# Performance work log

Hardware: AMD Instinct MI355X
Metric: run time of the kernel (lower is better)

## Reference

```python
import jax, jax.numpy as jnp
import numpy as np

B, C_IN, C_OUT, L = 16, 128, 128, 1024
DK, DV, H = 32, 32, 8
SCALE = DK ** (-0.5)


def setup_inputs() -> dict:
    key = jax.random.key(0)
    ks = jax.random.split(key, 7)
    qkv_dim = H * (2 * DK + DV)
    # Conv1d with kernel_size=1 == per-position linear; store weights as (out, in)
    return {
        "x": jax.random.normal(ks[0], (B, C_IN, L), dtype=jnp.float32),
        "w_qkv": jax.random.normal(ks[1], (qkv_dim, C_IN), dtype=jnp.float32) * (C_IN ** -0.5),
        "b_qkv": jax.random.normal(ks[2], (qkv_dim,), dtype=jnp.float32) * 0.02,
        "w_o": jax.random.normal(ks[3], (C_OUT, H * DV), dtype=jnp.float32) * ((H * DV) ** -0.5),
        "b_o": jax.random.normal(ks[4], (C_OUT,), dtype=jnp.float32) * 0.02,
        "w_res": jax.random.normal(ks[5], (C_OUT, C_IN), dtype=jnp.float32) * (C_IN ** -0.5),
        "b_res": jax.random.normal(ks[6], (C_OUT,), dtype=jnp.float32) * 0.02,
    }


def reference(x, w_qkv, b_qkv, w_o, b_o, w_res, b_res):
    batch, _, seq = x.shape
    # qkv projection (1x1 conv): (B, H*(2dk+dv), L)
    qkv = jnp.einsum("oc,bcl->bol", w_qkv, x) + b_qkv[:, None]
    qkv = qkv.reshape(batch, H, 2 * DK + DV, seq)
    q = qkv[:, :, :DK]                 # (B, H, dk, L)
    k = qkv[:, :, DK:2 * DK]           # (B, H, dk, L)
    v = qkv[:, :, 2 * DK:]             # (B, H, dv, L)
    # logits = scale * q^T k : (B, H, L, L)
    logits = SCALE * jnp.einsum("bhds,bhdt->bhst", q, k)
    weights = jax.nn.softmax(logits, axis=-1)
    # z_i = (weights @ v^T)^T : (B, H, dv, L)
    z = jnp.einsum("bhst,bhdt->bhds", weights, v)
    z = z.reshape(batch, H * DV, seq)
    out = jnp.einsum("oc,bcl->bol", w_o, z) + b_o[:, None]
    out = out + jnp.einsum("oc,bcl->bol", w_res, x) + b_res[:, None]
    return out
```

## Files before the change

### kernel.cpp

```cpp
#include <hip/hip_runtime.h>

#define B_    16
#define L_    1024
#define H_    8
#define QSCALE 0.25510940349191965f

typedef __attribute__((ext_vector_type(8))) short bf16x8;
typedef __attribute__((ext_vector_type(4))) float f32x4;
typedef unsigned short u16t;

__device__ inline u16t f2bf(float f) {
    unsigned u = __float_as_uint(f);
    u = (u + 0x7FFF + ((u >> 16) & 1)) >> 16;
    return (u16t)u;
}
__device__ inline unsigned f2bf_pk(float a, float b) {
    unsigned ua = __float_as_uint(a);
    unsigned ub = __float_as_uint(b);
    ua = (ua + 0x7FFF + ((ua >> 16) & 1)) >> 16;
    ub = (ub + 0x7FFF + ((ub >> 16) & 1)) >> 16;
    return ua | (ub << 16);
}
__device__ inline uint2 f2bf_pk4(float a, float b, float c, float d) {
    uint2 u; u.x = f2bf_pk(a, b); u.y = f2bf_pk(c, d); return u;
}
__device__ inline unsigned trunc_pk(float f0, float f1) {
    return __builtin_amdgcn_perm(__float_as_uint(f1), __float_as_uint(f0), 0x07060302u);
}
__device__ inline void async16(const u16t* g, u16t* l) {
    __builtin_amdgcn_global_load_lds(
        (const __attribute__((address_space(1))) unsigned int*)g,
        (__attribute__((address_space(3))) unsigned int*)l, 16, 0, 0);
}

__global__ __launch_bounds__(256) void prep_kernel(
    const float* __restrict__ x, const float* __restrict__ w_qkv,
    const float* __restrict__ w_o, const float* __restrict__ w_res,
    u16t* __restrict__ xbT, u16t* __restrict__ wqb,
    u16t* __restrict__ wob, u16t* __restrict__ wrb)
{
    const int tid = threadIdx.x;
    if (blockIdx.z == 0) {
        __shared__ u16t T[64][144];
        const int b = blockIdx.y, l0 = blockIdx.x * 64;
#pragma unroll
        for (int i = 0; i < 8; i++) {
            const int c = i * 16 + (tid >> 4);
            const int l = (tid & 15) * 4;
            const float4 v = *(const float4*)(x + ((long)b * 128 + c) * 1024 + l0 + l);
            T[l + 0][c] = f2bf(v.x);
            T[l + 1][c] = f2bf(v.y);
            T[l + 2][c] = f2bf(v.z);
            T[l + 3][c] = f2bf(v.w);
        }
        __syncthreads();
#pragma unroll
        for (int i = 0; i < 4; i++) {
            const int l  = i * 16 + (tid >> 4);
            const int c0 = (tid & 15) * 8;
            *(uint4*)(xbT + ((long)b * 1024 + l0 + l) * 128 + c0) = *(const uint4*)&T[l][c0];
        }
    } else {
        const int idx = blockIdx.y * 16 + blockIdx.x;
        if (idx >= 144) return;
        const int f = idx * 1024 + tid * 4;
        const float* src; u16t* dst; int off;
        if (f < 98304)       { src = w_qkv; dst = wqb; off = f; }
        else if (f < 131072) { src = w_o;   dst = wob; off = f - 98304; }
        else                 { src = w_res; dst = wrb; off = f - 131072; }
        const float4 v = *(const float4*)(src + off);
        *(uint2*)(dst + off) = f2bf_pk4(v.x, v.y, v.z, v.w);
    }
}

__global__ __launch_bounds__(256) void qkv_gemm_kernel(
    const u16t* __restrict__ wqb, const u16t* __restrict__ xbT,
    const float* __restrict__ b_qkv,
    u16t* __restrict__ qT, u16t* __restrict__ kF, u16t* __restrict__ vF)
{
    __shared__ __align__(16) u16t Ws[96 * 136];

    const int lblk = blockIdx.x * 128;
    const int bh = blockIdx.y;
    const int b = bh >> 3, h = bh & 7;
    const int tid = threadIdx.x, lane = tid & 63, wv = tid >> 6;
    const int l15 = lane & 15, quad = lane >> 4;
    const int lw = lblk + wv * 32;

    {
        const u16t* wsrc = wqb + (long)h * 96 * 128;
#pragma unroll
        for (int i = 0; i < 6; i++) {
            const int g = tid + i * 256;
            const int row = g >> 4, col = g & 15;
            const uint4 w = *(const uint4*)(wsrc + g * 8);
            *(uint4*)&Ws[row * 136 + col * 8] = w;
        }
    }

    bf16x8 bfr[4][2];
    {
        const u16t* xr0 = xbT + ((long)b * 1024 + lw + l15) * 128 + quad * 8;
        const u16t* xr1 = xr0 + 16 * 128;
#pragma unroll
        for (int ks = 0; ks < 4; ks++) {
            bfr[ks][0] = *(const bf16x8*)(xr0 + ks * 32);
            bfr[ks][1] = *(const bf16x8*)(xr1 + ks * 32);
        }
    }
    __syncthreads();

    f32x4 acc[6][2];
#pragma unroll
    for (int mi = 0; mi < 6; mi++)
#pragma unroll
        for (int ni = 0; ni < 2; ni++) acc[mi][ni] = (f32x4)0.f;

#pragma unroll
    for (int ks = 0; ks < 4; ks++) {
#pragma unroll
        for (int mi = 0; mi < 6; mi++) {
            const bf16x8 af = *(const bf16x8*)&Ws[(mi * 16 + l15) * 136 + ks * 32 + quad * 8];
            acc[mi][0] = __builtin_amdgcn_mfma_f32_16x16x32_bf16(af, bfr[ks][0], acc[mi][0], 0, 0, 0);
            acc[mi][1] = __builtin_amdgcn_mfma_f32_16x16x32_bf16(af, bfr[ks][1], acc[mi][1], 0, 0, 0);
        }
    }

    const long bh_ = bh;
#pragma unroll
    for (int mi = 0; mi < 6; mi++) {
        float bias[4];
#pragma unroll
        for (int r = 0; r < 4; r++) bias[r] = b_qkv[h * 96 + mi * 16 + quad * 4 + r];
#pragma unroll
        for (int ni = 0; ni < 2; ni++) {
            const int l = lw + ni * 16 + l15;
            const f32x4 a = acc[mi][ni];
            if (mi < 2) {
                const uint2 u = f2bf_pk4((a[0] + bias[0]) * QSCALE, (a[1] + bias[1]) * QSCALE,
                                         (a[2] + bias[2]) * QSCALE, (a[3] + bias[3]) * QSCALE);
                *(uint2*)(qT + (bh_ * 1024 + l) * 32 + mi * 16 + quad * 4) = u;
            } else if (mi < 4) {
                const int t = l, c = t >> 6, tl = t & 63;
                const int qd = (mi - 2) * 2 + (quad >> 1);
                const uint2 u = f2bf_pk4(a[0] + bias[0], a[1] + bias[1],
                                         a[2] + bias[2], a[3] + bias[3]);
                *(uint2*)(kF + (bh_ * 16 + c) * 2048 + qd * 512 + tl * 8 + (quad & 1) * 4) = u;
            } else {
                const int t = l, c = t >> 6, tq = (t >> 3) & 7, j = t & 7;
                u16t* vb = vF + (bh_ * 16 + c) * 2048 + tq * 256 + j;
#pragma unroll
                for (int r = 0; r < 4; r++)
                    vb[((mi - 4) * 16 + quad * 4 + r) * 8] = f2bf(a[r] + bias[r]);
            }
        }
    }
}

__global__ __launch_bounds__(256) void attn_kernel8(
    const u16t* __restrict__ qT, const u16t* __restrict__ kF,
    const u16t* __restrict__ vF, u16t* __restrict__ zT)
{
    __shared__ __align__(16) u16t Ks[2][2048];
    __shared__ __align__(16) u16t Vs[2][2048];
    __shared__ __align__(16) u16t Ps[4][2][2][16][40];

    const int bh = blockIdx.x;
    const int b = bh >> 3, h = bh & 7;
    const int sblk = blockIdx.y * 128;
    const int tid = threadIdx.x, lane = tid & 63, wv = tid >> 6;
    const int l15 = lane & 15, quad = lane >> 4;

    const int sw = sblk + wv * 32;
    bf16x8 qf[2];
    qf[0] = *(const bf16x8*)(qT + ((long)bh * 1024 + sw + l15) * 32 + quad * 8);
    qf[1] = *(const bf16x8*)(qT + ((long)bh * 1024 + sw + 16 + l15) * 32 + quad * 8);

    const u16t* kg = kF + (long)bh * 32768 + tid * 8;
    const u16t* vg = vF + (long)bh * 32768 + tid * 8;

    async16(kg, &Ks[0][tid * 8]);
    async16(vg, &Vs[0][tid * 8]);

    f32x4 zacc[2][2];
#pragma unroll
    for (int a = 0; a < 2; a++)
#pragma unroll
        for (int c = 0; c < 2; c++) zacc[a][c] = (f32x4)0.f;
    f32x4 lacc4[2] = {(f32x4)0.f, (f32x4)0.f};

    for (int c = 0; c < 16; ++c) {
        const int buf = c & 1;
        __syncthreads();
        if (c < 15) {
            async16(kg + (c + 1) * 2048, &Ks[buf ^ 1][tid * 8]);
            async16(vg + (c + 1) * 2048, &Vs[buf ^ 1][tid * 8]);
        }

        bf16x8 kf[4];
#pragma unroll
        for (int tg = 0; tg < 4; tg++)
            kf[tg] = *(const bf16x8*)&Ks[buf][quad * 512 + (tg * 16 + l15) * 8];

#pragma unroll
        for (int st = 0; st < 2; st++) {
#pragma unroll
            for (int tg = 0; tg < 4; tg++) {
                const f32x4 sv = __builtin_amdgcn_mfma_f32_16x16x32_bf16(kf[tg], qf[st], (f32x4)0.f, 0, 0, 0);
                f32x4 ev;
#pragma unroll
                for (int i = 0; i < 4; i++) ev[i] = __builtin_amdgcn_exp2f(sv[i]);
                lacc4[st] += ev;
                uint2 u;
                u.x = trunc_pk(ev[0], ev[1]);
                u.y = trunc_pk(ev[2], ev[3]);
                *(uint2*)&Ps[wv][st][tg >> 1][l15][(tg & 1) * 16 + quad * 4] = u;
            }
        }

#pragma unroll
        for (int st = 0; st < 2; st++) {
#pragma unroll
            for (int tt = 0; tt < 2; tt++) {
                const bf16x8 pf  = *(const bf16x8*)&Ps[wv][st][tt][l15][quad * 8];
                const bf16x8 vf0 = *(const bf16x8*)&Vs[buf][(tt * 4 + quad) * 256 + l15 * 8];
                const bf16x8 vf1 = *(const bf16x8*)&Vs[buf][(tt * 4 + quad) * 256 + (16 + l15) * 8];
                zacc[st][0] = __builtin_amdgcn_mfma_f32_16x16x32_bf16(vf0, pf, zacc[st][0], 0, 0, 0);
                zacc[st][1] = __builtin_amdgcn_mfma_f32_16x16x32_bf16(vf1, pf, zacc[st][1], 0, 0, 0);
            }
        }
    }

#pragma unroll
    for (int st = 0; st < 2; st++) {
        float lf = (lacc4[st][0] + lacc4[st][1]) + (lacc4[st][2] + lacc4[st][3]);
        lf += __shfl_xor(lf, 16);
        lf += __shfl_xor(lf, 32);
        const float rl = 1.f / lf;
        const int s = sblk + wv * 32 + st * 16 + l15;
        u16t* zrow = zT + ((long)b * 1024 + s) * 256 + h * 32;
        const uint2 u0 = f2bf_pk4(zacc[st][0][0] * rl, zacc[st][0][1] * rl,
                                  zacc[st][0][2] * rl, zacc[st][0][3] * rl);
        *(uint2*)(zrow + quad * 4) = u0;
        const uint2 u1 = f2bf_pk4(zacc[st][1][0] * rl, zacc[st][1][1] * rl,
                                  zacc[st][1][2] * rl, zacc[st][1][3] * rl);
        *(uint2*)(zrow + 16 + quad * 4) = u1;
    }
}

__global__ __launch_bounds__(256, 4) void out_gemm_kernel(
    const u16t* __restrict__ wob, const u16t* __restrict__ wrb,
    const u16t* __restrict__ zT, const u16t* __restrict__ xbT,
    const float* __restrict__ b_o, const float* __restrict__ b_res,
    float* __restrict__ out)
{
    const int lblk = blockIdx.x * 32, oblk = blockIdx.y * 64, b = blockIdx.z;
    const int tid = threadIdx.x, lane = tid & 63, wv = tid >> 6;
    const int wm = wv >> 1, wn = wv & 1;
    const int l15 = lane & 15, quad = lane >> 4;
    const int ow = oblk + wm * 32;
    const int lw = lblk + wn * 16;

    f32x4 acc0 = (f32x4)0.f, acc1 = (f32x4)0.f;

    const u16t* zrow = zT + ((long)b * 1024 + lw + l15) * 256 + quad * 8;
    const u16t* xrow = xbT + ((long)b * 1024 + lw + l15) * 128 + quad * 8;
    const u16t* wo0 = wob + (ow + l15) * 256 + quad * 8;
    const u16t* wo1 = wob + (ow + 16 + l15) * 256 + quad * 8;
    const u16t* wr0 = wrb + (ow + l15) * 128 + quad * 8;
    const u16t* wr1 = wrb + (ow + 16 + l15) * 128 + quad * 8;

    bf16x8 af0[2], af1[2], bf[2];
    af0[0] = *(const bf16x8*)(wo0);
    af1[0] = *(const bf16x8*)(wo1);
    bf[0]  = *(const bf16x8*)(zrow);

#pragma unroll
    for (int ks = 0; ks < 12; ks++) {
        const int cur = ks & 1, nxt = cur ^ 1;
        if (ks < 11) {
            const int kn = ks + 1;
            if (kn < 8) {
                af0[nxt] = *(const bf16x8*)(wo0 + kn * 32);
                af1[nxt] = *(const bf16x8*)(wo1 + kn * 32);
                bf[nxt]  = *(const bf16x8*)(zrow + kn * 32);
            } else {
                af0[nxt] = *(const bf16x8*)(wr0 + (kn - 8) * 32);
                af1[nxt] = *(const bf16x8*)(wr1 + (kn - 8) * 32);
                bf[nxt]  = *(const bf16x8*)(xrow + (kn - 8) * 32);
            }
        }
        acc0 = __builtin_amdgcn_mfma_f32_16x16x32_bf16(af0[cur], bf[cur], acc0, 0, 0, 0);
        acc1 = __builtin_amdgcn_mfma_f32_16x16x32_bf16(af1[cur], bf[cur], acc1, 0, 0, 0);
    }

    const int lcol = lw + l15;
#pragma unroll
    for (int mi = 0; mi < 2; mi++) {
        const f32x4 a = (mi == 0) ? acc0 : acc1;
#pragma unroll
        for (int r = 0; r < 4; r++) {
            const int o = ow + mi * 16 + quad * 4 + r;
            out[((long)b * 128 + o) * 1024 + lcol] = a[r] + b_o[o] + b_res[o];
        }
    }
}

extern "C" void kernel_launch(void* const* d_in, const int* in_sizes, int n_in,
                              void* d_out, int out_size, void* d_ws, size_t ws_size,
                              hipStream_t stream)
{
    const float* x     = (const float*)d_in[0];
    const float* w_qkv = (const float*)d_in[1];
    const float* b_qkv = (const float*)d_in[2];
    const float* w_o   = (const float*)d_in[3];
    const float* b_o   = (const float*)d_in[4];
    const float* w_res = (const float*)d_in[5];
    const float* b_res = (const float*)d_in[6];
    float* out = (float*)d_out;

    u16t* xbT = (u16t*)d_ws;
    u16t* qT  = xbT + (size_t)2097152;
    u16t* kF  = qT  + (size_t)4194304;
    u16t* vF  = kF  + (size_t)4194304;
    u16t* zT  = vF  + (size_t)4194304;
    u16t* wqb = zT  + (size_t)4194304;
    u16t* wob = wqb + (size_t)98304;
    u16t* wrb = wob + (size_t)32768;

    prep_kernel<<<dim3(16, 16, 2), 256, 0, stream>>>(x, w_qkv, w_o, w_res, xbT, wqb, wob, wrb);
    qkv_gemm_kernel<<<dim3(8, 128, 1), 256, 0, stream>>>(wqb, xbT, b_qkv, qT, kF, vF);
    attn_kernel8<<<dim3(128, 8, 1), 256, 0, stream>>>(qT, kF, vF, zT);
    out_gemm_kernel<<<dim3(32, 2, 16), 256, 0, stream>>>(wob, wrb, zT, xbT, b_o, b_res, out);
}
```

Measured before the change: 136.3 us.

## Fuse weight bf16 conversion into GEMMs and double attention block size

Removes the separate weight-conversion blocks from the prep kernel. The QKV and output GEMMs now load fp32 weights and convert them to bf16 in shared memory, and the output GEMM stages its weights in LDS. The attention kernel moves to 512 threads covering 256 query rows per block, so each K/V chunk load is shared by twice as many waves, with K and V loads split across thread halves. This trades redundant per-block weight conversion and larger blocks (fewer blocks, 512 in total) for less workspace traffic and fewer K/V reloads.

```diff
diff --git a/kernel.cpp b/kernel.cpp
--- a/kernel.cpp
+++ b/kernel.cpp
@@ -34,47 +34,32 @@
 }
 
 __global__ __launch_bounds__(256) void prep_kernel(
-    const float* __restrict__ x, const float* __restrict__ w_qkv,
-    const float* __restrict__ w_o, const float* __restrict__ w_res,
-    u16t* __restrict__ xbT, u16t* __restrict__ wqb,
-    u16t* __restrict__ wob, u16t* __restrict__ wrb)
-{
+    const float* __restrict__ x, u16t* __restrict__ xbT)
+{
+    __shared__ u16t T[64][144];
     const int tid = threadIdx.x;
-    if (blockIdx.z == 0) {
-        __shared__ u16t T[64][144];
-        const int b = blockIdx.y, l0 = blockIdx.x * 64;
-#pragma unroll
-        for (int i = 0; i < 8; i++) {
-            const int c = i * 16 + (tid >> 4);
-            const int l = (tid & 15) * 4;
-            const float4 v = *(const float4*)(x + ((long)b * 128 + c) * 1024 + l0 + l);
-            T[l + 0][c] = f2bf(v.x);
-            T[l + 1][c] = f2bf(v.y);
-            T[l + 2][c] = f2bf(v.z);
-            T[l + 3][c] = f2bf(v.w);
-        }
-        __syncthreads();
-#pragma unroll
-        for (int i = 0; i < 4; i++) {
-            const int l  = i * 16 + (tid >> 4);
-            const int c0 = (tid & 15) * 8;
-            *(uint4*)(xbT + ((long)b * 1024 + l0 + l) * 128 + c0) = *(const uint4*)&T[l][c0];
-        }
-    } else {
-        const int idx = blockIdx.y * 16 + blockIdx.x;
-        if (idx >= 144) return;
-        const int f = idx * 1024 + tid * 4;
-        const float* src; u16t* dst; int off;
-        if (f < 98304)       { src = w_qkv; dst = wqb; off = f; }
-        else if (f < 131072) { src = w_o;   dst = wob; off = f - 98304; }
-        else                 { src = w_res; dst = wrb; off = f - 131072; }
-        const float4 v = *(const float4*)(src + off);
-        *(uint2*)(dst + off) = f2bf_pk4(v.x, v.y, v.z, v.w);
+    const int b = blockIdx.y, l0 = blockIdx.x * 64;
+#pragma unroll
+    for (int i = 0; i < 8; i++) {
+        const int c = i * 16 + (tid >> 4);
+        const int l = (tid & 15) * 4;
+        const float4 v = *(const float4*)(x + ((long)b * 128 + c) * 1024 + l0 + l);
+        T[l + 0][c] = f2bf(v.x);
+        T[l + 1][c] = f2bf(v.y);
+        T[l + 2][c] = f2bf(v.z);
+        T[l + 3][c] = f2bf(v.w);
+    }
+    __syncthreads();
+#pragma unroll
+    for (int i = 0; i < 4; i++) {
+        const int l  = i * 16 + (tid >> 4);
+        const int c0 = (tid & 15) * 8;
+        *(uint4*)(xbT + ((long)b * 1024 + l0 + l) * 128 + c0) = *(const uint4*)&T[l][c0];
     }
 }
 
 __global__ __launch_bounds__(256) void qkv_gemm_kernel(
-    const u16t* __restrict__ wqb, const u16t* __restrict__ xbT,
+    const float* __restrict__ w_qkv, const u16t* __restrict__ xbT,
     const float* __restrict__ b_qkv,
     u16t* __restrict__ qT, u16t* __restrict__ kF, u16t* __restrict__ vF)
 {
@@ -88,13 +73,13 @@
     const int lw = lblk + wv * 32;
 
     {
-        const u16t* wsrc = wqb + (long)h * 96 * 128;
-#pragma unroll
-        for (int i = 0; i < 6; i++) {
-            const int g = tid + i * 256;
-            const int row = g >> 4, col = g & 15;
-            const uint4 w = *(const uint4*)(wsrc + g * 8);
-            *(uint4*)&Ws[row * 136 + col * 8] = w;
+        const float* wsrc = w_qkv + (long)h * 96 * 128;
+#pragma unroll
+        for (int it = 0; it < 12; it++) {
+            const int g = tid * 4 + it * 1024;
+            const int row = g >> 7, col = g & 127;
+            const float4 w = *(const float4*)(wsrc + g);
+            *(uint2*)&Ws[row * 136 + col] = f2bf_pk4(w.x, w.y, w.z, w.w);
         }
     }
 
@@ -157,17 +142,17 @@
     }
 }
 
-__global__ __launch_bounds__(256) void attn_kernel8(
+__global__ __launch_bounds__(512) void attn_kernel9(
     const u16t* __restrict__ qT, const u16t* __restrict__ kF,
     const u16t* __restrict__ vF, u16t* __restrict__ zT)
 {
     __shared__ __align__(16) u16t Ks[2][2048];
     __shared__ __align__(16) u16t Vs[2][2048];
-    __shared__ __align__(16) u16t Ps[4][2][2][16][40];
+    __shared__ __align__(16) u16t Ps[8][2][2][16][40];
 
     const int bh = blockIdx.x;
     const int b = bh >> 3, h = bh & 7;
-    const int sblk = blockIdx.y * 128;
+    const int sblk = blockIdx.y * 256;
     const int tid = threadIdx.x, lane = tid & 63, wv = tid >> 6;
     const int l15 = lane & 15, quad = lane >> 4;
 
@@ -176,11 +161,11 @@
     qf[0] = *(const bf16x8*)(qT + ((long)bh * 1024 + sw + l15) * 32 + quad * 8);
     qf[1] = *(const bf16x8*)(qT + ((long)bh * 1024 + sw + 16 + l15) * 32 + quad * 8);
 
-    const u16t* kg = kF + (long)bh * 32768 + tid * 8;
-    const u16t* vg = vF + (long)bh * 32768 + tid * 8;
-
-    async16(kg, &Ks[0][tid * 8]);
-    async16(vg, &Vs[0][tid * 8]);
+    const u16t* kg = kF + (long)bh * 32768;
+    const u16t* vg = vF + (long)bh * 32768;
+
+    if (tid < 256) async16(kg + tid * 8, &Ks[0][tid * 8]);
+    else           async16(vg + (tid - 256) * 8, &Vs[0][(tid - 256) * 8]);
 
     f32x4 zacc[2][2];
 #pragma unroll
@@ -193,8 +178,9 @@
         const int buf = c & 1;
         __syncthreads();
         if (c < 15) {
-            async16(kg + (c + 1) * 2048, &Ks[buf ^ 1][tid * 8]);
-            async16(vg + (c + 1) * 2048, &Vs[buf ^ 1][tid * 8]);
+            const int o = (c + 1) * 2048;
+            if (tid < 256) async16(kg + o + tid * 8, &Ks[buf ^ 1][tid * 8]);
+            else           async16(vg + o + (tid - 256) * 8, &Vs[buf ^ 1][(tid - 256) * 8]);
         }
 
         bf16x8 kf[4];
@@ -248,12 +234,15 @@
     }
 }
 
-__global__ __launch_bounds__(256, 4) void out_gemm_kernel(
-    const u16t* __restrict__ wob, const u16t* __restrict__ wrb,
+__global__ __launch_bounds__(256) void out_gemm_kernel(
+    const float* __restrict__ w_o, const float* __restrict__ w_res,
     const u16t* __restrict__ zT, const u16t* __restrict__ xbT,
     const float* __restrict__ b_o, const float* __restrict__ b_res,
     float* __restrict__ out)
 {
+    __shared__ __align__(16) u16t Wo[64 * 264];
+    __shared__ __align__(16) u16t Wr[64 * 136];
+
     const int lblk = blockIdx.x * 32, oblk = blockIdx.y * 64, b = blockIdx.z;
     const int tid = threadIdx.x, lane = tid & 63, wv = tid >> 6;
     const int wm = wv >> 1, wn = wv & 1;
@@ -261,37 +250,47 @@
     const int ow = oblk + wm * 32;
     const int lw = lblk + wn * 16;
 
+#pragma unroll
+    for (int it = 0; it < 16; it++) {
+        const int g = tid * 4 + it * 1024;
+        const int row = g >> 8, col = g & 255;
+        const float4 w = *(const float4*)(w_o + (long)(oblk + row) * 256 + col);
+        *(uint2*)&Wo[row * 264 + col] = f2bf_pk4(w.x, w.y, w.z, w.w);
+    }
+#pragma unroll
+    for (int it = 0; it < 8; it++) {
+        const int g = tid * 4 + it * 1024;
+        const int row = g >> 7, col = g & 127;
+        const float4 w = *(const float4*)(w_res + (long)(oblk + row) * 128 + col);
+        *(uint2*)&Wr[row * 136 + col] = f2bf_pk4(w.x, w.y, w.z, w.w);
+    }
+
+    bf16x8 bfz[8], bfx[4];
+    {
+        const u16t* zrow = zT + ((long)b * 1024 + lw + l15) * 256 + quad * 8;
+        const u16t* xrow = xbT + ((long)b * 1024 + lw + l15) * 128 + quad * 8;
+#pragma unroll
+        for (int ks = 0; ks < 8; ks++) bfz[ks] = *(const bf16x8*)(zrow + ks * 32);
+#pragma unroll
+        for (int ks = 0; ks < 4; ks++) bfx[ks] = *(const bf16x8*)(xrow + ks * 32);
+    }
+    __syncthreads();
+
     f32x4 acc0 = (f32x4)0.f, acc1 = (f32x4)0.f;
 
-    const u16t* zrow = zT + ((long)b * 1024 + lw + l15) * 256 + quad * 8;
-    const u16t* xrow = xbT + ((long)b * 1024 + lw + l15) * 128 + quad * 8;
-    const u16t* wo0 = wob + (ow + l15) * 256 + quad * 8;
-    const u16t* wo1 = wob + (ow + 16 + l15) * 256 + quad * 8;
-    const u16t* wr0 = wrb + (ow + l15) * 128 + quad * 8;
-    const u16t* wr1 = wrb + (ow + 16 + l15) * 128 + quad * 8;
-
-    bf16x8 af0[2], af1[2], bf[2];
-    af0[0] = *(const bf16x8*)(wo0);
-    af1[0] = *(const bf16x8*)(wo1);
-    bf[0]  = *(const bf16x8*)(zrow);
-
-#pragma unroll
-    for (int ks = 0; ks < 12; ks++) {
-        const int cur = ks & 1, nxt = cur ^ 1;
-        if (ks < 11) {
-            const int kn = ks + 1;
-            if (kn < 8) {
-                af0[nxt] = *(const bf16x8*)(wo0 + kn * 32);
-                af1[nxt] = *(const bf16x8*)(wo1 + kn * 32);
-                bf[nxt]  = *(const bf16x8*)(zrow + kn * 32);
-            } else {
-                af0[nxt] = *(const bf16x8*)(wr0 + (kn - 8) * 32);
-                af1[nxt] = *(const bf16x8*)(wr1 + (kn - 8) * 32);
-                bf[nxt]  = *(const bf16x8*)(xrow + (kn - 8) * 32);
-            }
-        }
-        acc0 = __builtin_amdgcn_mfma_f32_16x16x32_bf16(af0[cur], bf[cur], acc0, 0, 0, 0);
-        acc1 = __builtin_amdgcn_mfma_f32_16x16x32_bf16(af1[cur], bf[cur], acc1, 0, 0, 0);
+#pragma unroll
+    for (int ks = 0; ks < 8; ks++) {
+        const bf16x8 af0 = *(const bf16x8*)&Wo[(wm * 32 + l15) * 264 + ks * 32 + quad * 8];
+        const bf16x8 af1 = *(const bf16x8*)&Wo[(wm * 32 + 16 + l15) * 264 + ks * 32 + quad * 8];
+        acc0 = __builtin_amdgcn_mfma_f32_16x16x32_bf16(af0, bfz[ks], acc0, 0, 0, 0);
+        acc1 = __builtin_amdgcn_mfma_f32_16x16x32_bf16(af1, bfz[ks], acc1, 0, 0, 0);
+    }
+#pragma unroll
+    for (int ks = 0; ks < 4; ks++) {
+        const bf16x8 af0 = *(const bf16x8*)&Wr[(wm * 32 + l15) * 136 + ks * 32 + quad * 8];
+        const bf16x8 af1 = *(const bf16x8*)&Wr[(wm * 32 + 16 + l15) * 136 + ks * 32 + quad * 8];
+        acc0 = __builtin_amdgcn_mfma_f32_16x16x32_bf16(af0, bfx[ks], acc0, 0, 0, 0);
+        acc1 = __builtin_amdgcn_mfma_f32_16x16x32_bf16(af1, bfx[ks], acc1, 0, 0, 0);
     }
 
     const int lcol = lw + l15;
@@ -324,12 +323,9 @@
     u16t* kF  = qT  + (size_t)4194304;
     u16t* vF  = kF  + (size_t)4194304;
     u16t* zT  = vF  + (size_t)4194304;
-    u16t* wqb = zT  + (size_t)4194304;
-    u16t* wob = wqb + (size_t)98304;
-    u16t* wrb = wob + (size_t)32768;
-
-    prep_kernel<<<dim3(16, 16, 2), 256, 0, stream>>>(x, w_qkv, w_o, w_res, xbT, wqb, wob, wrb);
-    qkv_gemm_kernel<<<dim3(8, 128, 1), 256, 0, stream>>>(wqb, xbT, b_qkv, qT, kF, vF);
-    attn_kernel8<<<dim3(128, 8, 1), 256, 0, stream>>>(qT, kF, vF, zT);
-    out_gemm_kernel<<<dim3(32, 2, 16), 256, 0, stream>>>(wob, wrb, zT, xbT, b_o, b_res, out);
-}
+
+    prep_kernel<<<dim3(16, 16), 256, 0, stream>>>(x, xbT);
+    qkv_gemm_kernel<<<dim3(8, 128), 256, 0, stream>>>(w_qkv, xbT, b_qkv, qT, kF, vF);
+    attn_kernel9<<<dim3(128, 4), 512, 0, stream>>>(qT, kF, vF, zT);
+    out_gemm_kernel<<<dim3(32, 2, 16), 256, 0, stream>>>(w_o, w_res, zT, xbT, b_o, b_res, out);
+}
```

Result: faster. 127.0 us (-6.8%).
